# Kernel optimization log

Hardware: AMD Instinct MI355X
Metric: run time of the kernel (lower is better)

The kernel has to match this reference:

```python
import jax, jax.numpy as jnp
import numpy as np

P = 2          # SamplesLoss p=2
BLUR = 0.05    # eps_final = BLUR**P = 0.0025
SCALING = 0.8  # annealing factor per iteration (on the blur scale)


def _cost(x, y):
    # geomloss cost for p=2: |x - y|^2 / 2, shape (N, M)
    x2 = jnp.sum(x * x, axis=-1)
    y2 = jnp.sum(y * y, axis=-1)
    return 0.5 * (x2[:, None] + y2[None, :] - 2.0 * (x @ y.T))


def _softmin(eps, C, h):
    # -eps * log sum_j exp(h_j - C_ij / eps); h already contains log-weights
    return -eps * jax.nn.logsumexp(h[None, :] - C / eps, axis=1)


def _eps_schedule(x, y):
    # geomloss scaling_parameters / epsilon_schedule with diameter from bounding box
    xn, yn = np.asarray(x), np.asarray(y)
    mins = np.minimum(xn.min(0), yn.min(0))
    maxs = np.maximum(xn.max(0), yn.max(0))
    diameter = float(np.linalg.norm(maxs - mins))
    eps_list = ([diameter ** P]
                + [float(np.exp(e)) for e in np.arange(P * np.log(diameter), P * np.log(BLUR), P * np.log(SCALING))]
                + [BLUR ** P])
    return eps_list


def _sinkhorn_divergence(x, y, eps_list):
    # Debiased Sinkhorn divergence S_eps(x, y), geomloss sinkhorn_tensorized
    N, M = x.shape[0], y.shape[0]
    sg = jax.lax.stop_gradient
    C_xy, C_yx = _cost(x, y), _cost(y, x)
    C_xx, C_yy = _cost(x, sg(x)), _cost(y, sg(y))  # geomloss detaches 2nd arg
    # The annealing loop runs with autograd disabled in geomloss:
    Cxy_, Cyx_, Cxx_, Cyy_ = sg(C_xy), sg(C_yx), sg(C_xx), sg(C_yy)
    a_log = jnp.full((N,), -np.log(N), dtype=x.dtype)  # log uniform weights
    b_log = jnp.full((M,), -np.log(M), dtype=y.dtype)
    e0 = eps_list[0]
    f_aa = _softmin(e0, Cxx_, a_log)
    g_bb = _softmin(e0, Cyy_, b_log)
    g_ab = _softmin(e0, Cyx_, a_log)
    f_ba = _softmin(e0, Cxy_, b_log)
    for eps in eps_list:  # fixed schedule, not a data-dim loop
        ft_ba = _softmin(eps, Cxy_, b_log + g_ab / eps)
        gt_ab = _softmin(eps, Cyx_, a_log + f_ba / eps)
        ft_aa = _softmin(eps, Cxx_, a_log + f_aa / eps)
        gt_bb = _softmin(eps, Cyy_, b_log + g_bb / eps)
        f_ba, g_ab = 0.5 * (f_ba + ft_ba), 0.5 * (g_ab + gt_ab)
        f_aa, g_bb = 0.5 * (f_aa + ft_aa), 0.5 * (g_bb + gt_bb)
    # Final extrapolation step (the only one geomloss differentiates through):
    eps = eps_list[-1]
    f_ba, g_ab = (_softmin(eps, C_xy, sg(b_log + g_ab / eps)),
                  _softmin(eps, C_yx, sg(a_log + f_ba / eps)))
    f_aa = _softmin(eps, C_xx, sg(a_log + f_aa / eps))
    g_bb = _softmin(eps, C_yy, sg(b_log + g_bb / eps))
    # scal with uniform weights == mean
    return jnp.mean(f_ba - f_aa) + jnp.mean(g_ab - g_bb)


def setup_inputs() -> dict:
    key = jax.random.key(0)
    kx, kt = jax.random.split(key)
    x = jax.random.normal(kx, (4096, 64), dtype=jnp.float32)
    target = jax.random.normal(kt, (4096, 64), dtype=jnp.float32)
    return {"x": x, "target": target}


def reference(x, target):
    eps_list = _eps_schedule(x, target)  # concrete schedule from data diameter
    return _sinkhorn_divergence(x, target, eps_list)
```

## Files before the change

kernel.cpp:

```cpp
#include <hip/hip_runtime.h>
#include <math.h>

#define NPTS 4096
#define DIM  64
#define MAX_ITERS 37

#define ALOG (-8.317766166719343f)
#define L2E  (1.4426950408889634f)
#define LN2  (0.6931471805599453f)

#if __has_builtin(__builtin_amdgcn_exp2f)
#define EXP2F(x) __builtin_amdgcn_exp2f(x)
#else
#define EXP2F(x) exp2f(x)
#endif
#if __has_builtin(__builtin_amdgcn_logf)
#define LOG2F(x) __builtin_amdgcn_logf(x)
#else
#define LOG2F(x) log2f(x)
#endif

typedef _Float16 f16x8 __attribute__((ext_vector_type(8)));
typedef float    f32x4 __attribute__((ext_vector_type(4)));

__global__ void minmax_part_kernel(const float* __restrict__ x,
                                   const float* __restrict__ y,
                                   float* __restrict__ partmn,
                                   float* __restrict__ partmx) {
    int t = threadIdx.x;
    int bid = blockIdx.x;
    int g0 = bid * 256 + t;
    const int total = NPTS * DIM;
    float mn = INFINITY, mx = -INFINITY;
    for (int g = g0; g < total; g += 128 * 256) {
        float v = x[g]; mn = fminf(mn, v); mx = fmaxf(mx, v);
        float w = y[g]; mn = fminf(mn, w); mx = fmaxf(mx, w);
    }
    __shared__ float smn[256], smx[256];
    smn[t] = mn; smx[t] = mx;
    __syncthreads();
    if (t < 64) {
        for (int q = 1; q < 4; q++) {
            mn = fminf(mn, smn[t + 64 * q]);
            mx = fmaxf(mx, smx[t + 64 * q]);
        }
        partmn[bid * 64 + t] = mn;
        partmx[bid * 64 + t] = mx;
    }
}

__global__ void schedule_kernel(const float* __restrict__ partmn,
                                const float* __restrict__ partmx,
                                int* __restrict__ hdr,
                                float* __restrict__ sched) {
    int d = threadIdx.x;
    float mn = INFINITY, mx = -INFINITY;
    for (int b = 0; b < 128; b++) {
        mn = fminf(mn, partmn[b * 64 + d]);
        mx = fmaxf(mx, partmx[b * 64 + d]);
    }
    float range = mx - mn;
    __shared__ float r2[64];
    r2[d] = range * range;
    __syncthreads();
    if (d == 0) {
        float ss = 0.f;
        for (int k = 0; k < 64; k++) ss += r2[k];
        float diam_f = sqrtf(ss);
        double diam = (double)diam_f;
        double start = 2.0 * log(diam);
        double stop  = 2.0 * log(0.05);
        double step  = 2.0 * log(0.8);
        int n_ar = (int)ceil((stop - start) / step);
        if (n_ar < 0) n_ar = 0;
        int n_eps = n_ar + 2;
        if (n_eps > 63) n_eps = 63;
        sched[0] = (float)(diam * diam);
        for (int k = 0; k < n_ar && (1 + k) < 63; k++)
            sched[1 + k] = (float)exp(start + step * (double)k);
        sched[n_eps - 1] = 0.0025f;
        for (int k = n_eps; k < 64; k++) sched[k] = 0.0025f;
        hdr[0] = n_eps;
    }
}

__global__ void sqnorm_kernel(const float* __restrict__ X, float* __restrict__ out) {
    int wave = (blockIdx.x * blockDim.x + threadIdx.x) >> 6;
    int lane = threadIdx.x & 63;
    if (wave >= NPTS) return;
    float v = X[wave * DIM + lane];
    float s = v * v;
    for (int o = 32; o > 0; o >>= 1) s += __shfl_xor(s, o, 64);
    if (lane == 0) out[wave] = s;
}

__global__ void cast_kernel(const float* __restrict__ x, const float* __restrict__ y,
                            _Float16* __restrict__ X16, _Float16* __restrict__ Y16) {
    int g = blockIdx.x * 256 + threadIdx.x;
    X16[g] = (_Float16)x[g];
    Y16[g] = (_Float16)y[g];
}

__global__ __launch_bounds__(256, 4) void pass_kernel(
        const _Float16* __restrict__ X16, const _Float16* __restrict__ Y16,
        const float* __restrict__ x2, const float* __restrict__ y2,
        float* __restrict__ F, float* __restrict__ H, float* __restrict__ P,
        const int* __restrict__ hdr, const float* __restrict__ sched, int t) {
    const int n_eps = hdr[0];
    if (t >= 0 && t > n_eps) return;

    int b = blockIdx.x;
    int mat = b >> 8, rb = (b >> 3) & 31, cs = b & 7;
    const _Float16* Am = (mat == 0 || mat == 2) ? X16 : Y16;
    const _Float16* Bm = (mat == 1 || mat == 2) ? X16 : Y16;
    int matc = (mat < 2) ? (1 - mat) : mat;
    const float* sqr = (mat == 0 || mat == 2) ? x2 : y2;
    const float* sqc = (matc == 0 || matc == 2) ? x2 : y2;

    __shared__ float hs[512];
    __shared__ _Float16 Bs[2][64][72];

    int tt = threadIdx.x;
    int c0 = cs * 512, r0 = rb * 128;

    if (t == -2) {
        float inv2i = L2E / sched[0];
        for (int r = tt; r < 512; r += 256)
            hs[r] = ALOG * L2E - 0.5f * sqc[c0 + r] * inv2i;
    } else if (t == -1) {
        for (int r = tt; r < 512; r += 256)
            hs[r] = H[mat * 4096 + c0 + r];
    } else {
        int pp = (t == 0) ? 1 : ((t - 1) & 1);
        const float* Pm = P + pp * 262144;
        const float* Ps = Pm + 131072;
        float epsp = sched[(t == 0) ? 0 : (t - 1)];
        float inv2c = L2E / sched[t];
        for (int r = tt; r < 512; r += 256) {
            int row = c0 + r;
            int base = (matc * 8) * NPTS + row;
            float M = -INFINITY;
#pragma unroll
            for (int q = 0; q < 8; q++) M = fmaxf(M, Pm[base + q * NPTS]);
            float S = 0.f;
#pragma unroll
            for (int q = 0; q < 8; q++)
                S += Ps[base + q * NPTS] * EXP2F(Pm[base + q * NPTS] - M);
            float sq = sqc[row];
            float res = 0.5f * sq - epsp * LN2 * (M + LOG2F(S));
            float fnew = (t == 0) ? res
                       : 0.5f * (F[((t - 1) & 1) * 16384 + matc * 4096 + row] + res);
            float h = ALOG * L2E + (fnew - 0.5f * sq) * inv2c;
            hs[r] = h;
            if (rb == 0) {
                F[(t & 1) * 16384 + matc * 4096 + row] = fnew;
                H[mat * 4096 + row] = h;
            }
        }
    }
    __syncthreads();
    if (t >= 0 && t >= n_eps) return;

    int idx = (t == -2) ? 0 : ((t == -1) ? n_eps - 1 : t);
    float inv2 = L2E / sched[idx];

    int wv = tt >> 6, lane = tt & 63, q = lane >> 4, lo = lane & 15;

    f16x8 a[2][2];
#pragma unroll
    for (int rt = 0; rt < 2; rt++) {
        const _Float16* ar = Am + (size_t)(r0 + wv * 32 + rt * 16 + lo) * DIM + q * 8;
        a[rt][0] = *(const f16x8*)ar;
        a[rt][1] = *(const f16x8*)(ar + 32);
    }

    int srow = tt >> 2, scol = (tt & 3) * 16;
    {
        const _Float16* src = Bm + (size_t)(c0 + srow) * DIM + scol;
        *(f16x8*)&Bs[0][srow][scol]     = *(const f16x8*)src;
        *(f16x8*)&Bs[0][srow][scol + 8] = *(const f16x8*)(src + 8);
    }

    float m[2][4], s[2][4];
#pragma unroll
    for (int rt = 0; rt < 2; rt++)
#pragma unroll
        for (int r = 0; r < 4; r++) { m[rt][r] = -INFINITY; s[rt][r] = 0.f; }

    for (int ct = 0; ct < 8; ct++) {
        __syncthreads();
        f16x8 n0, n1;
        if (ct < 7) {
            const _Float16* src = Bm + (size_t)(c0 + (ct + 1) * 64 + srow) * DIM + scol;
            n0 = *(const f16x8*)src;
            n1 = *(const f16x8*)(src + 8);
        }
        const _Float16 (*Bt)[72] = Bs[ct & 1];
        float v[2][4][4];
#pragma unroll
        for (int cc = 0; cc < 4; cc++) {
            const _Float16* br = &Bt[cc * 16 + lo][q * 8];
            f16x8 b0 = *(const f16x8*)br;
            f16x8 b1 = *(const f16x8*)(br + 32);
            float hval = hs[ct * 64 + cc * 16 + lo];
#pragma unroll
            for (int rt = 0; rt < 2; rt++) {
                f32x4 acc = {0.f, 0.f, 0.f, 0.f};
                acc = __builtin_amdgcn_mfma_f32_16x16x32_f16(a[rt][0], b0, acc, 0, 0, 0);
                acc = __builtin_amdgcn_mfma_f32_16x16x32_f16(a[rt][1], b1, acc, 0, 0, 0);
#pragma unroll
                for (int r = 0; r < 4; r++) v[rt][r][cc] = fmaf(acc[r], inv2, hval);
            }
        }
#pragma unroll
        for (int rt = 0; rt < 2; rt++)
#pragma unroll
            for (int r = 0; r < 4; r++) {
                float lm = fmaxf(fmaxf(v[rt][r][0], v[rt][r][1]),
                                 fmaxf(v[rt][r][2], v[rt][r][3]));
                if (lm > m[rt][r] - 26.0f) {
                    float nm = fmaxf(m[rt][r], lm);
                    float acc = s[rt][r] * EXP2F(m[rt][r] - nm);
                    acc += EXP2F(v[rt][r][0] - nm) + EXP2F(v[rt][r][1] - nm)
                         + EXP2F(v[rt][r][2] - nm) + EXP2F(v[rt][r][3] - nm);
                    m[rt][r] = nm; s[rt][r] = acc;
                }
            }
        if (ct < 7) {
            *(f16x8*)&Bs[(ct + 1) & 1][srow][scol]     = n0;
            *(f16x8*)&Bs[(ct + 1) & 1][srow][scol + 8] = n1;
        }
    }

#pragma unroll
    for (int off = 1; off < 16; off <<= 1) {
#pragma unroll
        for (int rt = 0; rt < 2; rt++)
#pragma unroll
            for (int r = 0; r < 4; r++) {
                float om = __shfl_xor(m[rt][r], off, 64);
                float os = __shfl_xor(s[rt][r], off, 64);
                float nm = fmaxf(m[rt][r], om);
                s[rt][r] = s[rt][r] * EXP2F(m[rt][r] - nm) + os * EXP2F(om - nm);
                m[rt][r] = nm;
            }
    }
    if (lo == 0) {
        int pw = (t == -1) ? (n_eps & 1) : ((t == -2) ? 1 : (t & 1));
        float* Pm = P + pw * 262144;
        float* Ps = Pm + 131072;
#pragma unroll
        for (int rt = 0; rt < 2; rt++)
#pragma unroll
            for (int r = 0; r < 4; r++) {
                int row = r0 + wv * 32 + rt * 16 + q * 4 + r;
                Pm[(mat * 8 + cs) * NPTS + row] = m[rt][r];
                Ps[(mat * 8 + cs) * NPTS + row] = s[rt][r];
            }
    }
}

__global__ void finalize_kernel(const float* __restrict__ P,
                                const float* __restrict__ x2, const float* __restrict__ y2,
                                const int* __restrict__ hdr, const float* __restrict__ sched,
                                float* __restrict__ out) {
    int n_eps = hdr[0];
    const float* Pm = P + (n_eps & 1) * 262144;
    const float* Ps = Pm + 131072;
    int g = blockIdx.x * 256 + threadIdx.x;
    int mat = g >> 12, row = g & 4095;
    float eps = sched[n_eps - 1];
    const float* sqr = (mat == 0 || mat == 2) ? x2 : y2;
    int base = (mat * 8) * NPTS + row;
    float M = -INFINITY;
#pragma unroll
    for (int q = 0; q < 8; q++) M = fmaxf(M, Pm[base + q * NPTS]);
    float S = 0.f;
#pragma unroll
    for (int q = 0; q < 8; q++) S += Ps[base + q * NPTS] * EXP2F(Pm[base + q * NPTS] - M);
    float res = 0.5f * sqr[row] - eps * LN2 * (M + LOG2F(S));
    float val = ((mat == 0 || mat == 1) ? res : -res) * (1.0f / NPTS);
    __shared__ float sh[256];
    sh[threadIdx.x] = val;
    __syncthreads();
    for (int o = 128; o > 0; o >>= 1) {
        if (threadIdx.x < o) sh[threadIdx.x] += sh[threadIdx.x + o];
        __syncthreads();
    }
    if (threadIdx.x == 0) atomicAdd(out, sh[0]);
}

extern "C" void kernel_launch(void* const* d_in, const int* in_sizes, int n_in,
                              void* d_out, int out_size, void* d_ws, size_t ws_size,
                              hipStream_t stream) {
    const float* x = (const float*)d_in[0];
    const float* y = (const float*)d_in[1];
    float* out = (float*)d_out;
    float* w = (float*)d_ws;

    int*   hdr   = (int*)w;
    float* sched = w + 16;
    float* pmn   = w + 80;
    float* pmx   = w + 8272;
    float* x2    = w + 16464;
    float* y2    = w + 20560;
    float* F     = w + 24656;
    float* H     = w + 57424;
    float* P     = w + 73808;
    _Float16* X16 = (_Float16*)(w + 598096);
    _Float16* Y16 = (_Float16*)(w + 729168);

    hipMemsetAsync(out, 0, sizeof(float), stream);

    hipLaunchKernelGGL(minmax_part_kernel, dim3(128), dim3(256), 0, stream, x, y, pmn, pmx);
    hipLaunchKernelGGL(schedule_kernel, dim3(1), dim3(64), 0, stream, pmn, pmx, hdr, sched);
    hipLaunchKernelGGL(sqnorm_kernel, dim3(1024), dim3(256), 0, stream, x, x2);
    hipLaunchKernelGGL(sqnorm_kernel, dim3(1024), dim3(256), 0, stream, y, y2);
    hipLaunchKernelGGL(cast_kernel, dim3(1024), dim3(256), 0, stream, x, y, X16, Y16);

    hipLaunchKernelGGL(pass_kernel, dim3(1024), dim3(256), 0, stream,
                       X16, Y16, x2, y2, F, H, P, hdr, sched, -2);
    for (int t = 0; t < MAX_ITERS; t++)
        hipLaunchKernelGGL(pass_kernel, dim3(1024), dim3(256), 0, stream,
                           X16, Y16, x2, y2, F, H, P, hdr, sched, t);
    hipLaunchKernelGGL(pass_kernel, dim3(1024), dim3(256), 0, stream,
                       X16, Y16, x2, y2, F, H, P, hdr, sched, -1);

    hipLaunchKernelGGL(finalize_kernel, dim3(64), dim3(256), 0, stream,
                       P, x2, y2, hdr, sched, out);
}
```

Measured before the change: 979.2 us.

## Fuse all Sinkhorn passes into one persistent kernel with grid barriers

Replaces the sequence of about forty kernel launches (minmax, schedule, sqnorm, cast, per-iteration passes, finalize) with a single persistent mega-kernel that synchronises through a software sense-reversing grid barrier. The A-operand fragments are loaded into registers once and kept across all iterations, which removes per-launch overhead and the repeated A loads. Occupancy is queried at runtime to choose 1024 blocks or 512 blocks with two tiles each, falling back to the old multi-launch path otherwise. The risks are barrier spin cost, the deadlock hazard if not all blocks are co-resident, and higher register pressure.

Result: no change. 970.9 us (-0.8%).

```diff
diff --git a/kernel.cpp b/kernel.cpp
--- a/kernel.cpp
+++ b/kernel.cpp
@@ -22,6 +22,304 @@
 
 typedef _Float16 f16x8 __attribute__((ext_vector_type(8)));
 typedef float    f32x4 __attribute__((ext_vector_type(4)));
+
+__device__ __forceinline__ void grid_barrier(int* hdr, int* lsense) {
+    __syncthreads();
+    if (threadIdx.x == 0) {
+        int s = *lsense ^ 1;
+        __threadfence();
+        int prev = __hip_atomic_fetch_add(hdr + 4, 1, __ATOMIC_ACQ_REL,
+                                          __HIP_MEMORY_SCOPE_AGENT);
+        if (prev == (int)gridDim.x - 1) {
+            __hip_atomic_store(hdr + 4, 0, __ATOMIC_RELAXED, __HIP_MEMORY_SCOPE_AGENT);
+            __hip_atomic_store(hdr + 8, s, __ATOMIC_RELEASE, __HIP_MEMORY_SCOPE_AGENT);
+        } else {
+            while (__hip_atomic_load(hdr + 8, __ATOMIC_ACQUIRE,
+                                     __HIP_MEMORY_SCOPE_AGENT) != s)
+                __builtin_amdgcn_s_sleep(16);
+        }
+        *lsense = s;
+        __threadfence();
+    }
+    __syncthreads();
+}
+
+template <int TPB>
+__global__ __launch_bounds__(256, (TPB == 1 ? 4 : 2)) void mega_kernel(
+        const float* __restrict__ x, const float* __restrict__ y,
+        _Float16* __restrict__ X16, _Float16* __restrict__ Y16,
+        float* __restrict__ x2, float* __restrict__ y2,
+        float* __restrict__ pmn, float* __restrict__ pmx,
+        int* hdr, float* __restrict__ sched,
+        float* __restrict__ F, float* __restrict__ H, float* __restrict__ P,
+        float* __restrict__ out)
+{
+    const int b  = blockIdx.x;
+    const int tt = threadIdx.x;
+    int lsense = 0;
+
+    __shared__ float hs[512];
+    __shared__ _Float16 Bs[2][64][72];
+
+    for (int g = b * 256 + tt; g < NPTS * DIM; g += gridDim.x * 256) {
+        float xv = x[g], yv = y[g];
+        X16[g] = (_Float16)xv;
+        Y16[g] = (_Float16)yv;
+        float sx = xv * xv, sy = yv * yv;
+        for (int o = 32; o > 0; o >>= 1) {
+            sx += __shfl_xor(sx, o, 64);
+            sy += __shfl_xor(sy, o, 64);
+        }
+        if ((tt & 63) == 0) { x2[g >> 6] = sx; y2[g >> 6] = sy; }
+    }
+    if (b < 128) {
+        float mn = INFINITY, mx = -INFINITY;
+        for (int gg = b * 256 + tt; gg < NPTS * DIM; gg += 128 * 256) {
+            float v = x[gg]; mn = fminf(mn, v); mx = fmaxf(mx, v);
+            float w = y[gg]; mn = fminf(mn, w); mx = fmaxf(mx, w);
+        }
+        float* smn = hs;
+        float* smx = (float*)&Bs[0][0][0];
+        smn[tt] = mn; smx[tt] = mx;
+        __syncthreads();
+        if (tt < 64) {
+            for (int qq = 1; qq < 4; qq++) {
+                mn = fminf(mn, smn[tt + 64 * qq]);
+                mx = fmaxf(mx, smx[tt + 64 * qq]);
+            }
+            pmn[b * 64 + tt] = mn;
+            pmx[b * 64 + tt] = mx;
+        }
+    }
+    grid_barrier(hdr, &lsense);
+
+    if (b == 0) {
+        float* r2 = hs;
+        if (tt < 64) {
+            float mn = INFINITY, mx = -INFINITY;
+            for (int bb = 0; bb < 128; bb++) {
+                mn = fminf(mn, pmn[bb * 64 + tt]);
+                mx = fmaxf(mx, pmx[bb * 64 + tt]);
+            }
+            float range = mx - mn;
+            r2[tt] = range * range;
+        }
+        __syncthreads();
+        if (tt == 0) {
+            float ss = 0.f;
+            for (int k = 0; k < 64; k++) ss += r2[k];
+            float diam_f = sqrtf(ss);
+            double diam = (double)diam_f;
+            double start = 2.0 * log(diam);
+            double stop  = 2.0 * log(0.05);
+            double step  = 2.0 * log(0.8);
+            int n_ar = (int)ceil((stop - start) / step);
+            if (n_ar < 0) n_ar = 0;
+            int ne = n_ar + 2;
+            if (ne > 63) ne = 63;
+            sched[0] = (float)(diam * diam);
+            for (int k = 0; k < n_ar && (1 + k) < 63; k++)
+                sched[1 + k] = (float)exp(start + step * (double)k);
+            sched[ne - 1] = 0.0025f;
+            for (int k = ne; k < 64; k++) sched[k] = 0.0025f;
+            hdr[0] = ne;
+        }
+    }
+    grid_barrier(hdr, &lsense);
+
+    const int n_eps = *(volatile int*)hdr;
+
+    const int wv = tt >> 6, lane = tt & 63, q = lane >> 4, lo = lane & 15;
+    const int srow = tt >> 2, scol = (tt & 3) * 16;
+
+    f16x8 a[TPB][2][2];
+#pragma unroll
+    for (int sub = 0; sub < TPB; sub++) {
+        const int bt = b + 512 * sub;
+        const int mat_ = bt >> 8, rb_ = (bt >> 3) & 31;
+        const _Float16* Am = (mat_ == 0 || mat_ == 2) ? X16 : Y16;
+        const int r0_ = rb_ * 128;
+#pragma unroll
+        for (int rt = 0; rt < 2; rt++) {
+            const _Float16* ar = Am + (size_t)(r0_ + wv * 32 + rt * 16 + lo) * DIM + q * 8;
+            a[sub][rt][0] = *(const f16x8*)ar;
+            a[sub][rt][1] = *(const f16x8*)(ar + 32);
+        }
+    }
+
+    for (int p = 0; p <= n_eps + 2; p++) {
+        const int t = (p == 0) ? -2 : (p == n_eps + 2) ? -1 : (p - 1);
+        const bool do_main = (t < 0) || (t < n_eps);
+
+#pragma unroll
+        for (int sub = 0; sub < TPB; sub++) {
+            const int bt = b + 512 * sub;
+            const int mat = bt >> 8, rb = (bt >> 3) & 31, cs = bt & 7;
+            const _Float16* Bm = (mat == 1 || mat == 2) ? X16 : Y16;
+            const int matc = (mat < 2) ? (1 - mat) : mat;
+            const float* sqc = (matc == 0 || matc == 2) ? x2 : y2;
+            const int c0 = cs * 512, r0 = rb * 128;
+            const _Float16* Bsrc0 = Bm + (size_t)(c0 + srow) * DIM + scol;
+
+            f16x8 t0a, t0b;
+            if (do_main) {
+                t0a = *(const f16x8*)Bsrc0;
+                t0b = *(const f16x8*)(Bsrc0 + 8);
+            }
+
+            if (t == -2) {
+                float inv2i = L2E / sched[0];
+                for (int r = tt; r < 512; r += 256)
+                    hs[r] = ALOG * L2E - 0.5f * sqc[c0 + r] * inv2i;
+            } else if (t == -1) {
+                for (int r = tt; r < 512; r += 256)
+                    hs[r] = H[mat * 4096 + c0 + r];
+            } else {
+                int pp = (t == 0) ? 1 : ((t - 1) & 1);
+                const float* Pm = P + pp * 262144;
+                const float* Ps = Pm + 131072;
+                float epsp = sched[(t == 0) ? 0 : (t - 1)];
+                float inv2c = L2E / sched[t];
+                for (int r = tt; r < 512; r += 256) {
+                    int row = c0 + r;
+                    int base = (matc * 8) * NPTS + row;
+                    float M = -INFINITY;
+#pragma unroll
+                    for (int qq = 0; qq < 8; qq++) M = fmaxf(M, Pm[base + qq * NPTS]);
+                    float S = 0.f;
+#pragma unroll
+                    for (int qq = 0; qq < 8; qq++)
+                        S += Ps[base + qq * NPTS] * EXP2F(Pm[base + qq * NPTS] - M);
+                    float sq = sqc[row];
+                    float res = 0.5f * sq - epsp * LN2 * (M + LOG2F(S));
+                    float fnew = (t == 0) ? res
+                               : 0.5f * (F[((t - 1) & 1) * 16384 + matc * 4096 + row] + res);
+                    float h = ALOG * L2E + (fnew - 0.5f * sq) * inv2c;
+                    hs[r] = h;
+                    if (rb == 0) {
+                        F[(t & 1) * 16384 + matc * 4096 + row] = fnew;
+                        H[mat * 4096 + row] = h;
+                    }
+                }
+            }
+
+            if (do_main) {
+                int idx = (t == -2) ? 0 : ((t == -1) ? n_eps - 1 : t);
+                float inv2 = L2E / sched[idx];
+
+                *(f16x8*)&Bs[0][srow][scol]     = t0a;
+                *(f16x8*)&Bs[0][srow][scol + 8] = t0b;
+
+                float m[2][4], s[2][4];
+#pragma unroll
+                for (int rt = 0; rt < 2; rt++)
+#pragma unroll
+                    for (int r = 0; r < 4; r++) { m[rt][r] = -INFINITY; s[rt][r] = 0.f; }
+
+                for (int ct = 0; ct < 8; ct++) {
+                    __syncthreads();
+                    f16x8 n0, n1;
+                    if (ct < 7) {
+                        const _Float16* src = Bsrc0 + (size_t)(ct + 1) * 64 * DIM;
+                        n0 = *(const f16x8*)src;
+                        n1 = *(const f16x8*)(src + 8);
+                    }
+                    const _Float16 (*Bt)[72] = Bs[ct & 1];
+                    float v[2][4][4];
+#pragma unroll
+                    for (int cc = 0; cc < 4; cc++) {
+                        const _Float16* br = &Bt[cc * 16 + lo][q * 8];
+                        f16x8 b0 = *(const f16x8*)br;
+                        f16x8 b1 = *(const f16x8*)(br + 32);
+                        float hval = hs[ct * 64 + cc * 16 + lo];
+#pragma unroll
+                        for (int rt = 0; rt < 2; rt++) {
+                            f32x4 acc = {0.f, 0.f, 0.f, 0.f};
+                            acc = __builtin_amdgcn_mfma_f32_16x16x32_f16(a[sub][rt][0], b0, acc, 0, 0, 0);
+                            acc = __builtin_amdgcn_mfma_f32_16x16x32_f16(a[sub][rt][1], b1, acc, 0, 0, 0);
+#pragma unroll
+                            for (int r = 0; r < 4; r++) v[rt][r][cc] = fmaf(acc[r], inv2, hval);
+                        }
+                    }
+#pragma unroll
+                    for (int rt = 0; rt < 2; rt++)
+#pragma unroll
+                        for (int r = 0; r < 4; r++) {
+                            float lm = fmaxf(fmaxf(v[rt][r][0], v[rt][r][1]),
+                                             fmaxf(v[rt][r][2], v[rt][r][3]));
+                            if (lm > m[rt][r] - 26.0f) {
+                                float nm = fmaxf(m[rt][r], lm);
+                                float acc = s[rt][r] * EXP2F(m[rt][r] - nm);
+                                acc += EXP2F(v[rt][r][0] - nm) + EXP2F(v[rt][r][1] - nm)
+                                     + EXP2F(v[rt][r][2] - nm) + EXP2F(v[rt][r][3] - nm);
+                                m[rt][r] = nm; s[rt][r] = acc;
+                            }
+                        }
+                    if (ct < 7) {
+                        *(f16x8*)&Bs[(ct + 1) & 1][srow][scol]     = n0;
+                        *(f16x8*)&Bs[(ct + 1) & 1][srow][scol + 8] = n1;
+                    }
+                }
+
+#pragma unroll
+                for (int off = 1; off < 16; off <<= 1) {
+#pragma unroll
+                    for (int rt = 0; rt < 2; rt++)
+#pragma unroll
+                        for (int r = 0; r < 4; r++) {
+                            float om = __shfl_xor(m[rt][r], off, 64);
+                            float os = __shfl_xor(s[rt][r], off, 64);
+                            float nm = fmaxf(m[rt][r], om);
+                            s[rt][r] = s[rt][r] * EXP2F(m[rt][r] - nm) + os * EXP2F(om - nm);
+                            m[rt][r] = nm;
+                        }
+                }
+                if (lo == 0) {
+                    int pw = (t == -1) ? (n_eps & 1) : ((t == -2) ? 1 : (t & 1));
+                    float* Pw = P + pw * 262144;
+                    float* Sw = Pw + 131072;
+#pragma unroll
+                    for (int rt = 0; rt < 2; rt++)
+#pragma unroll
+                        for (int r = 0; r < 4; r++) {
+                            int row = r0 + wv * 32 + rt * 16 + q * 4 + r;
+                            Pw[(mat * 8 + cs) * NPTS + row] = m[rt][r];
+                            Sw[(mat * 8 + cs) * NPTS + row] = s[rt][r];
+                        }
+                }
+            }
+            __syncthreads();
+        }
+        grid_barrier(hdr, &lsense);
+    }
+
+    if (b < 64) {
+        const float* Pm = P + (n_eps & 1) * 262144;
+        const float* Ps = Pm + 131072;
+        int g = b * 256 + tt;
+        int fmat = g >> 12, row = g & 4095;
+        float eps = sched[n_eps - 1];
+        const float* sqr = (fmat == 0 || fmat == 2) ? x2 : y2;
+        int base = (fmat * 8) * NPTS + row;
+        float M = -INFINITY;
+#pragma unroll
+        for (int qq = 0; qq < 8; qq++) M = fmaxf(M, Pm[base + qq * NPTS]);
+        float S = 0.f;
+#pragma unroll
+        for (int qq = 0; qq < 8; qq++)
+            S += Ps[base + qq * NPTS] * EXP2F(Pm[base + qq * NPTS] - M);
+        float res = 0.5f * sqr[row] - eps * LN2 * (M + LOG2F(S));
+        float val = ((fmat < 2) ? res : -res) * (1.0f / NPTS);
+        float* sh = hs;
+        sh[tt] = val;
+        __syncthreads();
+        for (int o = 128; o > 0; o >>= 1) {
+            if (tt < o) sh[tt] += sh[tt + o];
+            __syncthreads();
+        }
+        if (tt == 0) atomicAdd(out, sh[0]);
+    }
+}
 
 __global__ void minmax_part_kernel(const float* __restrict__ x,
                                    const float* __restrict__ y,
@@ -114,7 +412,6 @@
     const _Float16* Am = (mat == 0 || mat == 2) ? X16 : Y16;
     const _Float16* Bm = (mat == 1 || mat == 2) ? X16 : Y16;
     int matc = (mat < 2) ? (1 - mat) : mat;
-    const float* sqr = (mat == 0 || mat == 2) ? x2 : y2;
     const float* sqc = (matc == 0 || matc == 2) ? x2 : y2;
 
     __shared__ float hs[512];
@@ -311,21 +608,32 @@
     _Float16* Y16 = (_Float16*)(w + 729168);
 
     hipMemsetAsync(out, 0, sizeof(float), stream);
-
-    hipLaunchKernelGGL(minmax_part_kernel, dim3(128), dim3(256), 0, stream, x, y, pmn, pmx);
-    hipLaunchKernelGGL(schedule_kernel, dim3(1), dim3(64), 0, stream, pmn, pmx, hdr, sched);
-    hipLaunchKernelGGL(sqnorm_kernel, dim3(1024), dim3(256), 0, stream, x, x2);
-    hipLaunchKernelGGL(sqnorm_kernel, dim3(1024), dim3(256), 0, stream, y, y2);
-    hipLaunchKernelGGL(cast_kernel, dim3(1024), dim3(256), 0, stream, x, y, X16, Y16);
-
-    hipLaunchKernelGGL(pass_kernel, dim3(1024), dim3(256), 0, stream,
-                       X16, Y16, x2, y2, F, H, P, hdr, sched, -2);
-    for (int t = 0; t < MAX_ITERS; t++)
+    hipMemsetAsync(hdr, 0, 64, stream);
+
+    int occ1 = 0, occ2 = 0;
+    (void)hipOccupancyMaxActiveBlocksPerMultiprocessor(&occ1, mega_kernel<1>, 256, 0);
+    (void)hipOccupancyMaxActiveBlocksPerMultiprocessor(&occ2, mega_kernel<2>, 256, 0);
+
+    if (occ1 >= 4) {
+        hipLaunchKernelGGL((mega_kernel<1>), dim3(1024), dim3(256), 0, stream,
+                           x, y, X16, Y16, x2, y2, pmn, pmx, hdr, sched, F, H, P, out);
+    } else if (occ2 >= 2) {
+        hipLaunchKernelGGL((mega_kernel<2>), dim3(512), dim3(256), 0, stream,
+                           x, y, X16, Y16, x2, y2, pmn, pmx, hdr, sched, F, H, P, out);
+    } else {
+        hipLaunchKernelGGL(minmax_part_kernel, dim3(128), dim3(256), 0, stream, x, y, pmn, pmx);
+        hipLaunchKernelGGL(schedule_kernel, dim3(1), dim3(64), 0, stream, pmn, pmx, hdr, sched);
+        hipLaunchKernelGGL(sqnorm_kernel, dim3(1024), dim3(256), 0, stream, x, x2);
+        hipLaunchKernelGGL(sqnorm_kernel, dim3(1024), dim3(256), 0, stream, y, y2);
+        hipLaunchKernelGGL(cast_kernel, dim3(1024), dim3(256), 0, stream, x, y, X16, Y16);
         hipLaunchKernelGGL(pass_kernel, dim3(1024), dim3(256), 0, stream,
-                           X16, Y16, x2, y2, F, H, P, hdr, sched, t);
-    hipLaunchKernelGGL(pass_kernel, dim3(1024), dim3(256), 0, stream,
-                       X16, Y16, x2, y2, F, H, P, hdr, sched, -1);
-
-    hipLaunchKernelGGL(finalize_kernel, dim3(64), dim3(256), 0, stream,
-                       P, x2, y2, hdr, sched, out);
-}
+                           X16, Y16, x2, y2, F, H, P, hdr, sched, -2);
+        for (int t = 0; t < MAX_ITERS; t++)
+            hipLaunchKernelGGL(pass_kernel, dim3(1024), dim3(256), 0, stream,
+                               X16, Y16, x2, y2, F, H, P, hdr, sched, t);
+        hipLaunchKernelGGL(pass_kernel, dim3(1024), dim3(256), 0, stream,
+                           X16, Y16, x2, y2, F, H, P, hdr, sched, -1);
+        hipLaunchKernelGGL(finalize_kernel, dim3(64), dim3(256), 0, stream,
+                           P, x2, y2, hdr, sched, out);
+    }
+}
```
